# Optimization experiments

Measured on AMD Instinct MI355X. Metric: run time of the kernel, lower is better.

Reference implementation:

```python
import jax, jax.numpy as jnp
import numpy as np

B, T, I, H, O = 128, 512, 64, 512, 1


def setup_inputs() -> dict:
    key = jax.random.key(0)
    ks = jax.random.split(key, 7)
    s = 1.0 / np.sqrt(H)  # torch default init scale
    return {
        "x": jax.random.normal(ks[0], (B, T, I), dtype=jnp.float32),
        "W_ih": jax.random.uniform(ks[1], (4 * H, I), jnp.float32, -s, s),
        "W_hh": jax.random.uniform(ks[2], (4 * H, H), jnp.float32, -s, s),
        "b_ih": jax.random.uniform(ks[3], (4 * H,), jnp.float32, -s, s),
        "b_hh": jax.random.uniform(ks[4], (4 * H,), jnp.float32, -s, s),
        "W_ho": jax.random.uniform(ks[5], (O, H), jnp.float32, -s, s),
        "b_ho": jax.random.uniform(ks[6], (O,), jnp.float32, -s, s),
    }


def reference(x, W_ih, W_hh, b_ih, b_hh, W_ho, b_ho):
    # Precompute input projections for all timesteps: [T, B, 4H]
    xg = jnp.einsum("bti,gi->tbg", x, W_ih) + b_ih + b_hh

    def step(carry, xg_t):
        h, c = carry
        gates = xg_t + h @ W_hh.T  # [B, 4H]
        i, f, g, o = jnp.split(gates, 4, axis=-1)  # torch LSTMCell gate order
        c = jax.nn.sigmoid(f) * c + jax.nn.sigmoid(i) * jnp.tanh(g)
        h = jax.nn.sigmoid(o) * jnp.tanh(c)
        return (h, c), h

    h0 = jnp.zeros((x.shape[0], W_hh.shape[1]), dtype=x.dtype)
    _, hs = jax.lax.scan(step, (h0, h0), xg)  # hs: [T, B, H]
    out = jnp.einsum("tbh,oh->bto", hs, W_ho) + b_ho  # [B, T, O]
    return out.squeeze(2)  # [B, T] since O == 1
```

## Files before the change

kernel.cpp:

```cpp
#include <hip/hip_runtime.h>


#define B_ 128
#define T_ 512
#define I_ 64
#define H_ 512

typedef __attribute__((ext_vector_type(8))) short short8;
typedef __attribute__((ext_vector_type(4))) float f32x4;
typedef __attribute__((ext_vector_type(4))) unsigned u32x4;

__device__ inline unsigned f2bf_u(float f) {
  union { float f; unsigned u; } v; v.f = f;
  return (v.u + 0x7fffu + ((v.u >> 16) & 1u)) >> 16;
}
__device__ inline float bf2f(unsigned s) {
  union { unsigned u; float f; } v; v.u = s << 16; return v.f;
}
__device__ inline float sigm(float x) { return 1.0f / (1.0f + __expf(-x)); }
__device__ inline float tanh_(float x) { return 1.0f - 2.0f / (1.0f + __expf(2.0f * x)); }

#define WAITV(N)                                        \
  asm volatile("s_waitcnt vmcnt(" #N ")" ::: "memory"); \
  __builtin_amdgcn_sched_barrier(0)

#define HLOADQ(dst, base, OFF)                                            \
  asm volatile("global_load_dwordx4 %0, %1, off offset:" #OFF " sc0 sc1"  \
               : "=v"(dst) : "v"(base))

#define XLOADQ(dst, base, OFF)                                            \
  asm volatile("global_load_dwordx4 %0, %1, off offset:" #OFF             \
               : "=v"(dst) : "v"(base))

#define HSTORED2(base, v64)                                               \
  asm volatile("global_store_dwordx2 %0, %1, off sc0 sc1"                 \
               :: "v"(base), "v"(v64) : "memory")

__global__ __launch_bounds__(256, 1) void lstm_kernel(
    const float* __restrict__ x,
    const float* __restrict__ Wih,
    const float* __restrict__ Whh,
    const float* __restrict__ bih,
    const float* __restrict__ bhh,
    const float* __restrict__ Who,
    float* __restrict__ part,
    unsigned short* __restrict__ hbuf,
    unsigned* __restrict__ flags)
{
  const int bid = blockIdx.x;
  const int jg = bid >> 3;
  const int bg = bid & 7;
  const int tid = threadIdx.x;
  const int w = tid >> 6;
  const int l = tid & 63;
  const int l16 = l & 15;
  const int lk = l >> 4;
  const int b = bg * 16 + l16;

  short8 a_hh[4][16], a_ih[4][2];
  float bias[4][4], who[4];
#pragma unroll
  for (int m = 0; m < 4; ++m) {
    const int rowA = w * 64 + m * 16 + l16;
    const int grow = (rowA & 3) * 512 + jg * 64 + (rowA >> 2);
#pragma unroll
    for (int kt = 0; kt < 16; ++kt) {
      const float* p = Whh + (size_t)grow * H_ + kt * 32 + lk * 8;
      short8 s;
#pragma unroll
      for (int e = 0; e < 8; ++e) s[e] = (short)f2bf_u(p[e]);
      a_hh[m][kt] = s;
    }
#pragma unroll
    for (int kt = 0; kt < 2; ++kt) {
      const float* p = Wih + (size_t)grow * I_ + kt * 32 + lk * 8;
      short8 s;
#pragma unroll
      for (int e = 0; e < 8; ++e) s[e] = (short)f2bf_u(p[e]);
      a_ih[m][kt] = s;
    }
    const int jm = jg * 64 + w * 16 + m * 4 + lk;
#pragma unroll
    for (int g = 0; g < 4; ++g) bias[m][g] = bih[g * 512 + jm] + bhh[g * 512 + jm];
    who[m] = Who[jm];
  }

  __shared__ unsigned short hlds[2][2][16][512];
#define HOFS(pl, bb, kt) (((((pl) * 16 + (bb)) * 512) + (kt) * 32 + lk * 8) ^ (((bb) & 7) << 3))

  unsigned short* const hb0 = hbuf;
  unsigned short* const hb1 = hbuf + 2 * B_ * H_;
  unsigned* const fbase = flags + (size_t)bg * 32;
  unsigned* const myflag = fbase + (jg * 4 + w);
  const float* const xrow = x + (size_t)b * (T_ * I_);

  float c[4] = {0.f, 0.f, 0.f, 0.f};
  f32x4 xf0, xf1, xf2, xf3;
  {
    const float* xb = xrow + lk * 8;
    XLOADQ(xf0, xb, 0);   XLOADQ(xf1, xb, 16);
    XLOADQ(xf2, xb, 128); XLOADQ(xf3, xb, 144);
    WAITV(0);
  }

  for (int t = 0; t < T_; ++t) {
    const int pr = t & 1;
    const unsigned short* hp = pr ? hb1 : hb0;
    unsigned short* hn       = pr ? hb0 : hb1;
    unsigned short* const hldsF = &hlds[pr][0][0][0];

    f32x4 acc[4][2];
#pragma unroll
    for (int m = 0; m < 4; ++m) {
      acc[m][0] = (f32x4){0.f, 0.f, 0.f, 0.f};
      acc[m][1] = (f32x4){0.f, 0.f, 0.f, 0.f};
    }

#pragma unroll
    for (int kt = 0; kt < 2; ++kt) {
      f32x4 va = kt ? xf2 : xf0;
      f32x4 vb = kt ? xf3 : xf1;
      float v[8] = {va[0], va[1], va[2], va[3], vb[0], vb[1], vb[2], vb[3]};
      short8 xhi, xlo;
#pragma unroll
      for (int e = 0; e < 8; ++e) {
        unsigned hb = f2bf_u(v[e]);
        xhi[e] = (short)hb;
        xlo[e] = (short)f2bf_u(v[e] - bf2f(hb));
      }
#pragma unroll
      for (int m = 0; m < 4; ++m) {
        acc[m][0] = __builtin_amdgcn_mfma_f32_16x16x32_bf16(a_ih[m][kt], xhi, acc[m][0], 0, 0, 0);
        acc[m][1] = __builtin_amdgcn_mfma_f32_16x16x32_bf16(a_ih[m][kt], xlo, acc[m][1], 0, 0, 0);
      }
    }

    if (t > 0) {
      {
        const unsigned* fp = fbase + (l & 31);
        for (;;) {
          unsigned f = __hip_atomic_load(fp, __ATOMIC_RELAXED, __HIP_MEMORY_SCOPE_AGENT);
          if (__all(f >= (unsigned)t)) break;
        }
      }
      __builtin_amdgcn_fence(__ATOMIC_ACQUIRE, "workgroup");
      __builtin_amdgcn_sched_barrier(0);

      u32x4 qh[4], ql[4];
      {
        const unsigned short* phh = hp + (size_t)b * H_ + w * 128 + lk * 8;
        const unsigned short* pll = phh + (size_t)(B_ * H_);
        HLOADQ(qh[0], phh, 0);   HLOADQ(qh[1], phh, 64);
        HLOADQ(qh[2], phh, 128); HLOADQ(qh[3], phh, 192);
        HLOADQ(ql[0], pll, 0);   HLOADQ(ql[1], pll, 64);
        HLOADQ(ql[2], pll, 128); HLOADQ(ql[3], pll, 192);
        const int tn = (t + 1 < T_) ? t + 1 : t;
        const float* xb = xrow + tn * I_ + lk * 8;
        XLOADQ(xf0, xb, 0);   XLOADQ(xf1, xb, 16);
        XLOADQ(xf2, xb, 128); XLOADQ(xf3, xb, 144);
      }
      WAITV(4);

#pragma unroll
      for (int i = 0; i < 4; ++i) {
        *(u32x4*)&hldsF[HOFS(0, l16, 4 * w + i)] = qh[i];
        *(u32x4*)&hldsF[HOFS(1, l16, 4 * w + i)] = ql[i];
      }
      __syncthreads();

#pragma unroll
      for (int kt = 0; kt < 16; ++kt) {
        short8 fh = *(const short8*)&hldsF[HOFS(0, l16, kt)];
        short8 fl = *(const short8*)&hldsF[HOFS(1, l16, kt)];
#pragma unroll
        for (int m = 0; m < 4; ++m) {
          acc[m][0] = __builtin_amdgcn_mfma_f32_16x16x32_bf16(a_hh[m][kt], fh, acc[m][0], 0, 0, 0);
          acc[m][1] = __builtin_amdgcn_mfma_f32_16x16x32_bf16(a_hh[m][kt], fl, acc[m][1], 0, 0, 0);
        }
      }
    } else {
      const float* xb = xrow + I_ + lk * 8;
      XLOADQ(xf0, xb, 0);   XLOADQ(xf1, xb, 16);
      XLOADQ(xf2, xb, 128); XLOADQ(xf3, xb, 144);
    }

    float p = 0.f;
    unsigned wd[4];
#pragma unroll
    for (int m = 0; m < 4; ++m) {
      float gi = sigm(acc[m][0].x + acc[m][1].x + bias[m][0]);
      float gf = sigm(acc[m][0].y + acc[m][1].y + bias[m][1]);
      float gg = tanh_(acc[m][0].z + acc[m][1].z + bias[m][2]);
      float go = sigm(acc[m][0].w + acc[m][1].w + bias[m][3]);
      c[m] = gf * c[m] + gi * gg;
      float hv = go * tanh_(c[m]);
      p += hv * who[m];
      unsigned hb = f2bf_u(hv);
      wd[m] = hb | (f2bf_u(hv - bf2f(hb)) << 16);
    }

    {
      unsigned r0[4], r1[4];
#pragma unroll
      for (int m = 0; m < 4; ++m) r0[m] = __shfl_xor(wd[m], 16);
#pragma unroll
      for (int m = 0; m < 4; ++m) if ((m ^ lk) & 1) wd[m] = r0[m ^ 1];
#pragma unroll
      for (int m = 0; m < 4; ++m) r1[m] = __shfl_xor(wd[m], 32);
#pragma unroll
      for (int m = 0; m < 4; ++m) if ((m ^ lk) & 2) wd[m] = r1[m ^ 2];
    }

    {
      unsigned hi01 = (wd[0] & 0xffffu) | (wd[1] << 16);
      unsigned hi23 = (wd[2] & 0xffffu) | (wd[3] << 16);
      unsigned lo01 = (wd[0] >> 16) | (wd[1] & 0xffff0000u);
      unsigned lo23 = (wd[2] >> 16) | (wd[3] & 0xffff0000u);
      unsigned long long hiq = (unsigned long long)hi01 | ((unsigned long long)hi23 << 32);
      unsigned long long loq = (unsigned long long)lo01 | ((unsigned long long)lo23 << 32);
      unsigned short* ph = hn + (size_t)b * H_ + jg * 64 + w * 16 + lk * 4;
      HSTORED2(ph, hiq);
      HSTORED2(ph + B_ * H_, loq);
    }

    WAITV(0);
    if (l == 0)
      __hip_atomic_store(myflag, (unsigned)(t + 1),
                         __ATOMIC_RELAXED, __HIP_MEMORY_SCOPE_AGENT);

    p += __shfl_xor(p, 16);
    p += __shfl_xor(p, 32);
    if (l < 16) atomicAdd(part + (size_t)b * T_ + t, p);
  }
#undef HOFS
}

__global__ __launch_bounds__(256) void reduce_out(const float* __restrict__ part,
                                                  const float* __restrict__ b_ho,
                                                  float* __restrict__ out) {
  int i = blockIdx.x * blockDim.x + threadIdx.x;
  if (i < B_ * T_) out[i] = part[i] + b_ho[0];
}

extern "C" void kernel_launch(void* const* d_in, const int* in_sizes, int n_in,
                              void* d_out, int out_size, void* d_ws, size_t ws_size,
                              hipStream_t stream) {
  (void)in_sizes; (void)n_in; (void)out_size; (void)ws_size;
  const float* x   = (const float*)d_in[0];
  const float* Wih = (const float*)d_in[1];
  const float* Whh = (const float*)d_in[2];
  const float* bih = (const float*)d_in[3];
  const float* bhh = (const float*)d_in[4];
  const float* Who = (const float*)d_in[5];
  const float* bho = (const float*)d_in[6];
  float* out = (float*)d_out;

  unsigned short* hbuf = (unsigned short*)d_ws;
  const size_t hbytes = (size_t)2 * 2 * B_ * H_ * sizeof(unsigned short);
  float* part = (float*)((char*)d_ws + hbytes);
  const size_t pbytes = (size_t)B_ * T_ * sizeof(float);
  unsigned* flags = (unsigned*)((char*)d_ws + hbytes + pbytes);

  hipMemsetAsync((char*)d_ws + hbytes, 0, pbytes + 8 * 32 * sizeof(unsigned), stream);

  lstm_kernel<<<dim3(64), dim3(256), 0, stream>>>(x, Wih, Whh, bih, bhh, Who,
                                                  part, hbuf, flags);
  reduce_out<<<(B_ * T_ + 255) / 256, 256, 0, stream>>>(part, bho, out);
}
```

Measured before the change: 2.523 ms.

## Embed timestep tags in h payload bits and poll data directly instead of flags

Encodes a small timestep tag into the low bits of the bf16 hi/lo h words written by lane group 0. Consumers spin on loading the h data itself until the tags match, so they no longer need to wait for the store to complete before setting a flag. The WAITV(0) before the flag store is removed. Partial outputs are now split per column group and summed in the reduce kernel, which cuts atomic contention. The cost is corrupting the two low mantissa bits of some h values, and the design depends on hi/lo tag visibility ordering, which is subtle. The old flag spin loop appears to still be present before the tag check.

```diff
diff --git a/kernel.cpp b/kernel.cpp
--- a/kernel.cpp
+++ b/kernel.cpp
@@ -109,6 +109,8 @@
     unsigned short* hn       = pr ? hb0 : hb1;
     unsigned short* const hldsF = &hlds[pr][0][0][0];
 
+    WAITV(4);
+
     f32x4 acc[4][2];
 #pragma unroll
     for (int m = 0; m < 4; ++m) {
@@ -147,19 +149,38 @@
       __builtin_amdgcn_sched_barrier(0);
 
       u32x4 qh[4], ql[4];
+      const unsigned short* phh = hp + (size_t)b * H_ + w * 128 + lk * 8;
+      const unsigned short* pll = phh + (size_t)(B_ * H_);
+      HLOADQ(qh[0], phh, 0);   HLOADQ(qh[1], phh, 64);
+      HLOADQ(qh[2], phh, 128); HLOADQ(qh[3], phh, 192);
+      HLOADQ(ql[0], pll, 0);   HLOADQ(ql[1], pll, 64);
+      HLOADQ(ql[2], pll, 128); HLOADQ(ql[3], pll, 192);
       {
-        const unsigned short* phh = hp + (size_t)b * H_ + w * 128 + lk * 8;
-        const unsigned short* pll = phh + (size_t)(B_ * H_);
+        const int tn = (t + 1 < T_) ? t + 1 : t;
+        const float* xb = xrow + tn * I_ + lk * 8;
+        XLOADQ(xf0, xb, 0);   XLOADQ(xf1, xb, 16);
+        XLOADQ(xf2, xb, 128); XLOADQ(xf3, xb, 144);
+      }
+      WAITV(4);
+
+      const unsigned tlo = (unsigned)(t & 3);
+      const unsigned thi = (unsigned)((t >> 2) & 3);
+      for (;;) {
+        unsigned bad = 0;
+#pragma unroll
+        for (int i = 0; i < 4; ++i) {
+          bad |= (qh[i].x ^ tlo) | (qh[i].z ^ thi)
+               | (ql[i].x ^ tlo) | (ql[i].z ^ thi);
+        }
+        bad &= 3u;
+        if (__all(bad == 0)) break;
         HLOADQ(qh[0], phh, 0);   HLOADQ(qh[1], phh, 64);
         HLOADQ(qh[2], phh, 128); HLOADQ(qh[3], phh, 192);
         HLOADQ(ql[0], pll, 0);   HLOADQ(ql[1], pll, 64);
         HLOADQ(ql[2], pll, 128); HLOADQ(ql[3], pll, 192);
-        const int tn = (t + 1 < T_) ? t + 1 : t;
-        const float* xb = xrow + tn * I_ + lk * 8;
-        XLOADQ(xf0, xb, 0);   XLOADQ(xf1, xb, 16);
-        XLOADQ(xf2, xb, 128); XLOADQ(xf3, xb, 144);
-      }
-      WAITV(4);
+        WAITV(0);
+      }
+      __builtin_amdgcn_sched_barrier(0);
 
 #pragma unroll
       for (int i = 0; i < 4; ++i) {
@@ -184,6 +205,7 @@
       XLOADQ(xf2, xb, 128); XLOADQ(xf3, xb, 144);
     }
 
+    const unsigned tgp = (unsigned)((t + 1) & 15);
     float p = 0.f;
     unsigned wd[4];
 #pragma unroll
@@ -195,8 +217,12 @@
       c[m] = gf * c[m] + gi * gg;
       float hv = go * tanh_(c[m]);
       p += hv * who[m];
+      unsigned tb = (m & 1) ? (tgp >> 2) : (tgp & 3u);
       unsigned hb = f2bf_u(hv);
-      wd[m] = hb | (f2bf_u(hv - bf2f(hb)) << 16);
+      if (lk == 0) hb = (hb & ~3u) | tb;
+      unsigned lo = f2bf_u(hv - bf2f(hb));
+      if (lk == 0) lo = (lo & ~3u) | tb;
+      wd[m] = hb | (lo << 16);
     }
 
     {
@@ -222,15 +248,13 @@
       HSTORED2(ph, hiq);
       HSTORED2(ph + B_ * H_, loq);
     }
-
-    WAITV(0);
     if (l == 0)
       __hip_atomic_store(myflag, (unsigned)(t + 1),
                          __ATOMIC_RELAXED, __HIP_MEMORY_SCOPE_AGENT);
 
     p += __shfl_xor(p, 16);
     p += __shfl_xor(p, 32);
-    if (l < 16) atomicAdd(part + (size_t)b * T_ + t, p);
+    if (l < 16) atomicAdd(part + ((size_t)jg * B_ + b) * T_ + t, p);
   }
 #undef HOFS
 }
@@ -239,7 +263,12 @@
                                                   const float* __restrict__ b_ho,
                                                   float* __restrict__ out) {
   int i = blockIdx.x * blockDim.x + threadIdx.x;
-  if (i < B_ * T_) out[i] = part[i] + b_ho[0];
+  if (i < B_ * T_) {
+    float s = b_ho[0];
+#pragma unroll
+    for (int g = 0; g < 8; ++g) s += part[(size_t)g * B_ * T_ + i];
+    out[i] = s;
+  }
 }
 
 extern "C" void kernel_launch(void* const* d_in, const int* in_sizes, int n_in,
@@ -258,7 +287,7 @@
   unsigned short* hbuf = (unsigned short*)d_ws;
   const size_t hbytes = (size_t)2 * 2 * B_ * H_ * sizeof(unsigned short);
   float* part = (float*)((char*)d_ws + hbytes);
-  const size_t pbytes = (size_t)B_ * T_ * sizeof(float);
+  const size_t pbytes = (size_t)8 * B_ * T_ * sizeof(float);
   unsigned* flags = (unsigned*)((char*)d_ws + hbytes + pbytes);
 
   hipMemsetAsync((char*)d_ws + hbytes, 0, pbytes + 8 * 32 * sizeof(unsigned), stream);
```

New measurement: 2.692 ms. +6.7%, slower.
